# Kernel tuning notes

Hardware: AMD Instinct MI355X
Metric: run time of the kernel (lower is better)

Reference implementation:

```python
import jax, jax.numpy as jnp
import numpy as np

N_HASHES = 4
CHUNK = 144
REDUCTION = 4

# PyTorch bicubic (a=-0.75), align_corners=False, integer scale 2 ->
# fixed fractional offsets t=0.75 (even outputs) and t=0.25 (odd outputs).
_EW = jnp.array([-0.03515625, 0.26171875, 0.87890625, -0.10546875], jnp.float32)
_OW = _EW[::-1]


def _up2_axis(x, axis):
    n = x.shape[axis]
    pad = [(0, 0)] * x.ndim
    pad[axis] = (2, 2)
    xp = jnp.pad(x, pad, mode='edge')  # torch clamps border indices
    sl = lambda s: jax.lax.slice_in_dim(xp, s, s + n, axis=axis)
    even = sum(_EW[k] * sl(k) for k in range(4))
    odd = sum(_OW[k] * sl(k + 1) for k in range(4))
    out = jnp.stack([even, odd], axis=axis + 1)
    shp = list(x.shape)
    shp[axis] = 2 * n
    return out.reshape(shp)


def bicubic_up2(x):
    return _up2_axis(_up2_axis(x, 2), 3)


def conv2d(x, w, b, pad):
    y = jax.lax.conv_general_dilated(x, w, (1, 1), [(pad, pad), (pad, pad)],
                                     dimension_numbers=('NCHW', 'OIHW', 'NCHW'))
    return y + b[None, :, None, None]


def _adj(t):
    # attend to own + two adjacent buckets along chunk axis (axis=2)
    return jnp.concatenate([t, jnp.roll(t, 1, axis=2), jnp.roll(t, -1, axis=2)], axis=3)


def nlsa(x, wm, bm, wa, ba, rot):
    N, Cc, H, W = x.shape
    L = H * W
    xe = conv2d(x, wm, bm, 1).reshape(N, -1, L).transpose(0, 2, 1)  # [N,L,C]
    ye = conv2d(x, wa, ba, 0).reshape(N, -1, L).transpose(0, 2, 1)  # [N,L,C*red]
    C = xe.shape[-1]
    hash_buckets = min(L // CHUNK + (L // CHUNK) % 2, 128)
    # LSH: random rotations -> argmax bucket codes (non-differentiable, detached)
    rotated = jnp.einsum('btf,fhi->bhti', xe, rot)  # [N,h,L,hb//2]
    rotated = jnp.concatenate([rotated, -rotated], axis=-1)  # [N,h,L,hb]
    codes = jnp.argmax(rotated, axis=-1)  # [N,h,L]
    codes = codes + (jnp.arange(N_HASHES) * hash_buckets)[None, :, None]
    codes = jax.lax.stop_gradient(codes.reshape(N, -1))  # [N,h*L]
    indices = jnp.argsort(codes, axis=-1)
    undo = jnp.argsort(indices, axis=-1)
    mod = indices % L
    xs = jnp.take_along_axis(xe, mod[..., None], axis=1)  # [N,h*L,C]
    ys = jnp.take_along_axis(ye, mod[..., None], axis=1)  # [N,h*L,C*red]
    padding = (-L) % CHUNK
    xb = xs.reshape(N, N_HASHES, L, C)
    yb = ys.reshape(N, N_HASHES, L, C * REDUCTION)
    if padding:
        xb = jnp.concatenate([xb, xb[:, :, -padding:, :]], axis=2)
        yb = jnp.concatenate([yb, yb[:, :, -padding:, :]], axis=2)
    nch = xb.shape[2] // CHUNK
    xb = xb.reshape(N, N_HASHES, nch, CHUNK, C)
    yb = yb.reshape(N, N_HASHES, nch, CHUNK, C * REDUCTION)
    xm = xb / jnp.maximum(jnp.linalg.norm(xb, axis=-1, keepdims=True), 5e-5)
    xm = _adj(xm)      # [N,h,k,3*chunk,C]
    ybj = _adj(yb)     # [N,h,k,3*chunk,C*red]
    raw = jnp.einsum('bhkie,bhkje->bhkij', xb, xm)  # [N,h,k,chunk,3*chunk]
    bscore = jax.scipy.special.logsumexp(raw, axis=-1, keepdims=True)
    score = jnp.exp(raw - bscore)
    ret = jnp.einsum('bhkij,bhkje->bhkie', score, ybj)
    ret = ret.reshape(N, N_HASHES, -1, C * REDUCTION)
    bscore = bscore.reshape(N, N_HASHES, -1)
    if padding:
        ret = ret[:, :, :-padding]
        bscore = bscore[:, :, :-padding]
    ret = ret.reshape(N, -1, C * REDUCTION)
    bscore = bscore.reshape(N, -1)
    ret = jnp.take_along_axis(ret, undo[..., None], axis=1)
    bscore = jnp.take_along_axis(bscore, undo, axis=1)
    ret = ret.reshape(N, N_HASHES, L, C * REDUCTION)
    probs = jax.nn.softmax(bscore.reshape(N, N_HASHES, L, 1), axis=1)
    ret = jnp.sum(ret * probs, axis=1)  # [N,L,C*red]
    return ret.transpose(0, 2, 1).reshape(N, -1, H, W) + x


def setup_inputs() -> dict:
    key = jax.random.key(0)
    ks = jax.random.split(key, 8)
    w = lambda k, shape, fan: (jax.random.normal(k, shape, jnp.float32) / np.sqrt(fan)).astype(jnp.float32)
    return {
        'x': jax.random.normal(ks[0], (2, 64, 96, 96), jnp.float32),
        'w1': w(ks[1], (64, 64, 3, 3), 64 * 9), 'b1': jnp.zeros((64,), jnp.float32),
        'w2': w(ks[2], (64, 64, 3, 3), 64 * 9), 'b2': jnp.zeros((64,), jnp.float32),
        'wm': w(ks[3], (16, 64, 3, 3), 64 * 9), 'bm': jnp.zeros((16,), jnp.float32),
        'wa': w(ks[4], (64, 64, 1, 1), 64), 'ba': jnp.zeros((64,), jnp.float32),
        'rot': jax.random.normal(ks[5], (16, N_HASHES, 64), jnp.float32),  # [C, h, hash_buckets//2]
    }


def reference(x, w1, b1, w2, b2, wm, bm, wa, ba, rot):
    x = bicubic_up2(x)
    x = jax.nn.relu(conv2d(x, w1, b1, 1))
    x = jax.nn.relu(conv2d(x, w2, b2, 1))
    return nlsa(x, wm, bm, wa, ba, rot)
```

## Files before the change

kernel.cpp:

```cpp
#include <hip/hip_runtime.h>
#include <math.h>

#define NB 2
#define CIN 64
#define H0 96
#define W0 96
#define HH 192
#define WW 192
#define LL (HH*WW)
#define NHASH 4
#define CHK 144
#define NCHK 256
#define CE 16
#define CV 64
#define NBUCK 128
#define SEGL 576
#define NSEG 64

#define K_ROWB   80
#define V_ROWB   912
#define P_ROWB   72
#define KQ_SZB   34560
#define VT_SZB   58368
#define PST_SZB  10368
#define LKI_SZB  1728
#define QN_SZB   576
#define LDS_T1   (VT_SZB + PST_SZB + LKI_SZB)
#define LDS_T2   (KQ_SZB + VT_SZB + PST_SZB + LKI_SZB + QN_SZB)

typedef __attribute__((ext_vector_type(8))) short short8_t;
typedef __attribute__((ext_vector_type(4))) float f32x4;
union FragU { unsigned int u[4]; int4 i; short8_t s; };

__device__ __forceinline__ unsigned int cvtpk_bf16(float a, float b){
  unsigned int r;
  asm("v_cvt_pk_bf16_f32 %0, %1, %2" : "=v"(r) : "v"(a), "v"(b));
  return r;
}
__device__ __forceinline__ float bfl(unsigned int u){ return __uint_as_float(u << 16); }
__device__ __forceinline__ float bfh(unsigned int u){ return __uint_as_float(u & 0xffff0000u); }

__global__ __launch_bounds__(256) void k_upsample(const float* __restrict__ x,
                                                  float* __restrict__ out){
  int idx = blockIdx.x*256 + threadIdx.x;
  if (idx >= NB*CIN*HH*WW) return;
  int ox = idx % WW; int t2 = idx / WW;
  int oy = t2 % HH;  t2 /= HH;
  int i = oy >> 1, a = oy & 1;
  int j = ox >> 1, b = ox & 1;
  const float e0=-0.03515625f, e1=0.26171875f, e2=0.87890625f, e3=-0.10546875f;
  float wy[4], wx[4]; int ty[4], tx[4];
  if (a){ wy[0]=e3; wy[1]=e2; wy[2]=e1; wy[3]=e0; } else { wy[0]=e0; wy[1]=e1; wy[2]=e2; wy[3]=e3; }
  if (b){ wx[0]=e3; wx[1]=e2; wx[2]=e1; wx[3]=e0; } else { wx[0]=e0; wx[1]=e1; wx[2]=e2; wx[3]=e3; }
  int offy = a ? -1 : -2, offx = b ? -1 : -2;
  #pragma unroll
  for (int k=0;k<4;k++){
    int t = i + offy + k; ty[k] = t<0?0:(t>H0-1?H0-1:t);
    int s = j + offx + k; tx[k] = s<0?0:(s>W0-1?W0-1:s);
  }
  const float* xp = x + (size_t)t2*H0*W0;
  float s = 0.f;
  #pragma unroll
  for (int ky=0;ky<4;ky++){
    const float* row = xp + ty[ky]*W0;
    float rs = 0.f;
    rs = fmaf(wx[0], row[tx[0]], rs);
    rs = fmaf(wx[1], row[tx[1]], rs);
    rs = fmaf(wx[2], row[tx[2]], rs);
    rs = fmaf(wx[3], row[tx[3]], rs);
    s = fmaf(wy[ky], rs, s);
  }
  out[idx] = s;
}

__global__ __launch_bounds__(256) void k_prepw(const float* __restrict__ w,
    unsigned short* __restrict__ wsT, int CO){
  int idx = blockIdx.x*256 + threadIdx.x;
  if (idx >= CO*64*9) return;
  int tap = idx % 9; int rem = idx / 9;
  int ci = rem % 64; int co = rem / 64;
  float v = w[(size_t)(co*64 + ci)*9 + tap];
  unsigned int hu = cvtpk_bf16(v, v) & 0xffffu;
  float hf = bfl(hu);
  unsigned int lu = cvtpk_bf16(v - hf, 0.f) & 0xffffu;
  int half = ci >> 5, kg = (ci >> 3) & 3, e = ci & 7;
  size_t base = ((size_t)(tap*2 + half)*2)*CO*32 + ((size_t)co*4 + kg)*8 + e;
  wsT[base]         = (unsigned short)hu;
  wsT[base + (size_t)CO*32] = (unsigned short)lu;
}

template<int CO, bool RELU, bool OUT_NLC>
__global__ __launch_bounds__(256) void k_conv3m(const float* __restrict__ in,
    const unsigned short* __restrict__ wsT, const float* __restrict__ bias,
    float* __restrict__ out){
  __shared__ unsigned short inH[3][66][64];
  __shared__ unsigned short inL[3][66][64];
  const int t = threadIdx.x;
  const int bx = blockIdx.x, y = blockIdx.y, n = blockIdx.z;
  const int x0 = bx*64;
  const int l = t & 63, w = t >> 6;
  const int lq = l & 15, kg = l >> 4;

  for (int e = t; e < 3072; e += 256){
    const int chunk = e & 15;
    const int strip = e >> 4;
    const int ci = strip & 63, row = strip >> 6;
    const int gy = y + row - 1;
    float4 v = make_float4(0.f,0.f,0.f,0.f);
    if (gy >= 0 && gy < HH)
      v = *(const float4*)&in[(((size_t)n*CIN + ci)*HH + gy)*WW + x0 + chunk*4];
    float vv[4] = {v.x, v.y, v.z, v.w};
    #pragma unroll
    for (int j = 0; j < 4; ++j){
      const int col = 1 + chunk*4 + j;
      const int sci = (((ci >> 3) ^ (col & 7)) << 3) | (ci & 7);
      unsigned int hu = cvtpk_bf16(vv[j], vv[j]);
      unsigned int lu = cvtpk_bf16(vv[j] - bfl(hu), 0.f);
      inH[row][col][sci] = (unsigned short)hu;
      inL[row][col][sci] = (unsigned short)lu;
    }
  }
  if (t < 192){
    const int ci = t & 63, row = t >> 6;
    const int gy = y + row - 1;
    const bool okY = (gy >= 0 && gy < HH);
    const float* ip = &in[(((size_t)n*CIN + ci)*HH + (size_t)(okY?gy:0))*WW];
    float vL = (okY && x0 >= 1) ? ip[x0-1] : 0.f;
    float vR = (okY && x0+64 < WW) ? ip[x0+64] : 0.f;
    unsigned int hL = cvtpk_bf16(vL, vL);
    unsigned int lLu = cvtpk_bf16(vL - bfl(hL), 0.f);
    unsigned int hR = cvtpk_bf16(vR, vR);
    unsigned int lRu = cvtpk_bf16(vR - bfl(hR), 0.f);
    const int sci0 = ci;
    const int sci65 = (((ci >> 3) ^ 1) << 3) | (ci & 7);
    inH[row][0][sci0]  = (unsigned short)hL;  inL[row][0][sci0]  = (unsigned short)lLu;
    inH[row][65][sci65] = (unsigned short)hR; inL[row][65][sci65] = (unsigned short)lRu;
  }
  __syncthreads();

  constexpr int NCT = CO/16;
  f32x4 acc[NCT];
  #pragma unroll
  for (int c=0;c<NCT;c++) acc[c] = (f32x4){0.f,0.f,0.f,0.f};
  const unsigned short* wlane = wsT + (size_t)lq*32 + (size_t)kg*8;

  #pragma unroll
  for (int tap=0; tap<9; ++tap){
    const int ky = tap/3, kx = tap - ky*3;
    const int col = w*16 + lq + kx;
    #pragma unroll
    for (int half=0; half<2; ++half){
      const int sci = ((((half<<2) | kg) ^ (col & 7)) << 3);
      FragU Bh, Bl;
      Bh.i = *(const int4*)&inH[ky][col][sci];
      Bl.i = *(const int4*)&inL[ky][col][sci];
      const unsigned short* wth = wlane + (size_t)((tap*2+half)*2)*CO*32;
      #pragma unroll
      for (int ct=0; ct<NCT; ++ct){
        FragU Ah, Al;
        Ah.i = *(const int4*)(wth + ct*512);
        Al.i = *(const int4*)(wth + CO*32 + ct*512);
        acc[ct] = __builtin_amdgcn_mfma_f32_16x16x32_bf16(Ah.s, Bl.s, acc[ct], 0,0,0);
        acc[ct] = __builtin_amdgcn_mfma_f32_16x16x32_bf16(Al.s, Bh.s, acc[ct], 0,0,0);
        acc[ct] = __builtin_amdgcn_mfma_f32_16x16x32_bf16(Ah.s, Bh.s, acc[ct], 0,0,0);
      }
    }
  }

  const int px = x0 + w*16 + lq;
  if constexpr (!OUT_NLC){
    #pragma unroll
    for (int ct=0; ct<NCT; ++ct){
      #pragma unroll
      for (int r=0; r<4; ++r){
        const int co = ct*16 + kg*4 + r;
        float v = acc[ct][r] + bias[co];
        if (RELU) v = fmaxf(v, 0.f);
        out[(((size_t)n*CO + co)*HH + y)*WW + px] = v;
      }
    }
  } else {
    #pragma unroll
    for (int r=0; r<4; ++r){
      const int co = kg*4 + r;
      float v = acc[0][r] + bias[co];
      if (RELU) v = fmaxf(v, 0.f);
      out[((size_t)n*LL + y*WW + px)*CO + co] = v;
    }
  }
}

__global__ __launch_bounds__(256) void k_conv1x1(const float* __restrict__ x2,
    const float* __restrict__ wa, const float* __restrict__ ba,
    unsigned short* __restrict__ yeB){
  __shared__ float xs[64][64];
  __shared__ float wts[64][64];
  const int t = threadIdx.x;
  const int n = blockIdx.y;
  const int l0 = blockIdx.x*64;
  for (int e=t; e<4096; e+=256){
    int ci = e >> 6, l = e & 63;
    xs[ci][l]  = x2[((size_t)n*CIN+ci)*LL + l0 + l];
    wts[ci][l] = wa[(size_t)l*64 + ci];
  }
  __syncthreads();
  const int l = t & 63, cq = t >> 6;
  float acc[16];
  #pragma unroll
  for (int i=0;i<16;i++) acc[i] = ba[cq*16+i];
  for (int ci=0; ci<64; ci++){
    float xv = xs[ci][l];
    #pragma unroll
    for (int i=0;i<16;i++) acc[i] = fmaf(xv, wts[ci][cq*16+i], acc[i]);
  }
  unsigned int wds[8];
  #pragma unroll
  for (int i=0;i<8;i++) wds[i] = cvtpk_bf16(acc[2*i], acc[2*i+1]);
  uint4* op = (uint4*)&yeB[((size_t)n*LL + l0 + l)*64 + cq*16];
  op[0] = make_uint4(wds[0],wds[1],wds[2],wds[3]);
  op[1] = make_uint4(wds[4],wds[5],wds[6],wds[7]);
}

__global__ __launch_bounds__(128) void k_codes(const float* __restrict__ xe,
    const float* __restrict__ rot, unsigned char* __restrict__ codes){
  __shared__ float rs[NHASH][64][16];
  const int t = threadIdx.x;
  for (int e=t; e<4096; e+=128){
    int f = e >> 8; int rem = e & 255;
    int h = rem >> 6; int i = rem & 63;
    rs[h][i][f] = rot[((size_t)f*NHASH + h)*64 + i];
  }
  __syncthreads();
  const int n = blockIdx.y;
  const int l = blockIdx.x*128 + t;
  float q[16];
  const float* xr = &xe[((size_t)n*LL + l)*16];
  #pragma unroll
  for (int f=0;f<16;f++) q[f] = xr[f];
  #pragma unroll
  for (int h=0;h<NHASH;h++){
    float bp = -3.0e38f, bn = -3.0e38f; int ap=0, an=0;
    for (int i=0;i<64;i++){
      float s = 0.f;
      #pragma unroll
      for (int f=0;f<16;f++) s = fmaf(q[f], rs[h][i][f], s);
      if (s > bp){ bp = s; ap = i; }
      if (-s > bn){ bn = -s; an = i; }
    }
    int code = (bp >= bn) ? ap : (64 + an);
    codes[((size_t)n*NHASH + h)*LL + l] = (unsigned char)code;
  }
}

__global__ __launch_bounds__(256) void k_hist(const unsigned char* __restrict__ codes,
    unsigned int* __restrict__ segHist){
  __shared__ unsigned int h[NBUCK];
  const int t = threadIdx.x;
  if (t < NBUCK) h[t] = 0;
  __syncthreads();
  const int n = blockIdx.z, hh = blockIdx.y, s = blockIdx.x;
  const unsigned char* cp = codes + ((size_t)n*NHASH + hh)*LL + (size_t)s*SEGL;
  for (int e=t; e<SEGL; e+=256) atomicAdd(&h[cp[e]], 1u);
  __syncthreads();
  if (t < NBUCK)
    segHist[(((size_t)(n*NHASH+hh))*NSEG + s)*NBUCK + t] = h[t];
}

__global__ __launch_bounds__(128) void k_scan(unsigned int* __restrict__ segHist){
  __shared__ unsigned int tot[NBUCK];
  __shared__ unsigned int base[NBUCK];
  const int b = threadIdx.x;
  const size_t off = (size_t)blockIdx.x * NSEG * NBUCK;
  unsigned int run = 0;
  for (int s=0;s<NSEG;s++){
    unsigned int v = segHist[off + (size_t)s*NBUCK + b];
    segHist[off + (size_t)s*NBUCK + b] = run;
    run += v;
  }
  tot[b] = run;
  __syncthreads();
  if (b==0){ unsigned int r=0; for (int i=0;i<NBUCK;i++){ base[i]=r; r+=tot[i]; } }
  __syncthreads();
  const unsigned int bb = base[b];
  for (int s=0;s<NSEG;s++) segHist[off + (size_t)s*NBUCK + b] += bb;
}

__global__ __launch_bounds__(256) void k_rank(const unsigned char* __restrict__ codes,
    const unsigned int* __restrict__ segHist, int* __restrict__ sortPos,
    int* __restrict__ srtIdx){
  __shared__ unsigned int cw[SEGL/4];
  __shared__ unsigned int sbase[NBUCK];
  const int t = threadIdx.x;
  const int n = blockIdx.z, hh = blockIdx.y, s = blockIdx.x;
  const size_t cb = ((size_t)n*NHASH + hh)*LL + (size_t)s*SEGL;
  const unsigned int* cp32 = (const unsigned int*)(codes + cb);
  for (int e=t; e<SEGL/4; e+=256) cw[e] = cp32[e];
  if (t < NBUCK)
    sbase[t] = segHist[(((size_t)(n*NHASH+hh))*NSEG + s)*NBUCK + t];
  __syncthreads();
  const size_t ob = ((size_t)n*NHASH + hh)*LL;
  for (int e=t; e<SEGL; e+=256){
    unsigned int c = (cw[e>>2] >> ((e&3)*8)) & 0xffu;
    unsigned int mul = c * 0x01010101u;
    int cnt = 0;
    const int nw = e >> 2;
    for (int wi=0; wi<nw; wi++){
      unsigned int v = cw[wi] ^ mul;
      unsigned int t1 = (v & 0x7f7f7f7fu) + 0x7f7f7f7fu;
      unsigned int z = ~(t1 | v) & 0x80808080u;
      cnt += __popc(z);
    }
    unsigned int lastw = cw[nw];
    const int nbp = e & 3;
    for (int bp=0; bp<nbp; bp++)
      if (((lastw >> (bp*8)) & 0xffu) == c) cnt++;
    int pos = (int)sbase[c] + cnt;
    int l = s*SEGL + e;
    sortPos[ob + l] = pos;
    srtIdx[ob + pos] = l;
  }
}

__global__ __launch_bounds__(256) void k_gatherK(const float* __restrict__ xe,
    const int* __restrict__ srtIdx, unsigned short* __restrict__ Ksrt,
    float* __restrict__ normQ){
  const int idx = blockIdx.x*256 + threadIdx.x;
  if (idx >= NB*NHASH*LL) return;
  const int n = idx / (NHASH*LL);
  const int lk = srtIdx[idx];
  const float4* xr = (const float4*)&xe[((size_t)n*LL + lk)*16];
  float4 v0 = xr[0], v1 = xr[1], v2 = xr[2], v3 = xr[3];
  float f[16] = {v0.x,v0.y,v0.z,v0.w, v1.x,v1.y,v1.z,v1.w,
                 v2.x,v2.y,v2.z,v2.w, v3.x,v3.y,v3.z,v3.w};
  float ss = 0.f;
  #pragma unroll
  for (int i=0;i<16;i++) ss = fmaf(f[i], f[i], ss);
  const float nq = sqrtf(ss);
  normQ[idx] = nq;
  const float inv = 1.f / fmaxf(nq, 5e-5f);
  #pragma unroll
  for (int i=0;i<16;i++) f[i] *= inv;
  unsigned int kh[8], klo[8];
  #pragma unroll
  for (int i=0;i<8;i++) kh[i] = cvtpk_bf16(f[2*i], f[2*i+1]);
  #pragma unroll
  for (int i=0;i<8;i++)
    klo[i] = cvtpk_bf16(f[2*i] - bfl(kh[i]), f[2*i+1] - bfh(kh[i]));
  int4* kr = (int4*)(Ksrt + (size_t)idx*32);
  kr[0] = make_int4((int)kh[0],(int)kh[1],(int)kh[2],(int)kh[3]);
  kr[1] = make_int4((int)kh[4],(int)kh[5],(int)kh[6],(int)kh[7]);
  kr[2] = make_int4((int)klo[0],(int)klo[1],(int)klo[2],(int)klo[3]);
  kr[3] = make_int4((int)klo[4],(int)klo[5],(int)klo[6],(int)klo[7]);
}

template<int TIER>
__global__ __launch_bounds__(576) void k_attn2(const float* __restrict__ xe,
    const unsigned short* __restrict__ yeB, const int* __restrict__ srtIdx,
    const unsigned short* __restrict__ Ksrt, const float* __restrict__ normQ,
    unsigned short* __restrict__ retS, float* __restrict__ bscore){
  extern __shared__ char smem[];
  constexpr int KQOFF = (TIER==2) ? KQ_SZB : 0;
  unsigned short* Kq = (unsigned short*)smem;
  char* Vt  = smem + KQOFF;
  char* Pst = Vt + VT_SZB;
  int* lkI  = (int*)(Pst + PST_SZB);
  float* qn = (float*)(Pst + PST_SZB + LKI_SZB);

  const int t = threadIdx.x;
  const int k = blockIdx.x, hh = blockIdx.y, n = blockIdx.z;
  const size_t sb = ((size_t)n*NHASH + hh)*LL;
  const int l = t & 63, w = t >> 6;
  const int lq16 = l & 15, g = l >> 4;

  if (t < 432){
    const int c3 = t / CHK, jl = t - c3*CHK;
    const int kc = (c3==0) ? k : ((c3==1) ? ((k+NCHK-1)&(NCHK-1)) : ((k+1)&(NCHK-1)));
    const int lk = srtIdx[sb + (size_t)kc*CHK + jl];
    lkI[t] = lk;
    if constexpr (TIER==2){
      const float4* xr = (const float4*)&xe[((size_t)n*LL + lk)*16];
      float4 v0 = xr[0], v1 = xr[1], v2 = xr[2], v3 = xr[3];
      float f[16] = {v0.x,v0.y,v0.z,v0.w, v1.x,v1.y,v1.z,v1.w,
                     v2.x,v2.y,v2.z,v2.w, v3.x,v3.y,v3.z,v3.w};
      float ss = 0.f;
      #pragma unroll
      for (int i=0;i<16;i++) ss = fmaf(f[i], f[i], ss);
      const float nq = sqrtf(ss);
      if (c3 == 0) qn[jl] = nq;
      const float inv = 1.f / fmaxf(nq, 5e-5f);
      #pragma unroll
      for (int i=0;i<16;i++) f[i] *= inv;
      unsigned int kh[8], klo[8];
      #pragma unroll
      for (int i=0;i<8;i++) kh[i] = cvtpk_bf16(f[2*i], f[2*i+1]);
      #pragma unroll
      for (int i=0;i<8;i++)
        klo[i] = cvtpk_bf16(f[2*i] - bfl(kh[i]), f[2*i+1] - bfh(kh[i]));
      int4* kr = (int4*)((char*)Kq + t*K_ROWB);
      kr[0] = make_int4((int)kh[0],(int)kh[1],(int)kh[2],(int)kh[3]);
      kr[1] = make_int4((int)kh[4],(int)kh[5],(int)kh[6],(int)kh[7]);
      kr[2] = make_int4((int)klo[0],(int)klo[1],(int)klo[2],(int)klo[3]);
      kr[3] = make_int4((int)klo[4],(int)klo[5],(int)klo[6],(int)klo[7]);
    }
  }
  if (t < 512){
    int c = t >> 3, jp = t & 7;
    *(unsigned int*)(Vt + c*V_ROWB + 864 + jp*4) = 0u;
  }
  __syncthreads();

  #pragma unroll 4
  for (int it=0; it<24; ++it){
    const int e = t + it*576;
    const int jp = e >> 6, c = e & 63;
    const unsigned int a = yeB[((size_t)n*LL + lkI[2*jp  ])*64 + c];
    const unsigned int b = yeB[((size_t)n*LL + lkI[2*jp+1])*64 + c];
    *(unsigned int*)(Vt + c*V_ROWB + jp*4) = a | (b << 16);
  }
  const int qg = w*16 + lq16;
  const int pq = k*CHK + qg;
  FragU b1, b2;
  float nq_;
  if constexpr (TIER==1){
    const unsigned short* qrow = Ksrt + (sb + pq)*32;
    b1.i = *(const int4*)(qrow + (g&1)*8);
    if (g < 2) b2.i = *(const int4*)(qrow + 16 + (g&1)*8);
    else { b2.u[0]=0u; b2.u[1]=0u; b2.u[2]=0u; b2.u[3]=0u; }
    nq_ = normQ[sb + pq];
  } else {
    const char* qrow = (const char*)Kq + qg*K_ROWB;
    b1.i = *(const int4*)(qrow + (g&1)*16);
    if (g < 2) b2.i = *(const int4*)(qrow + 32 + (g&1)*16);
    else { b2.u[0]=0u; b2.u[1]=0u; b2.u[2]=0u; b2.u[3]=0u; }
    nq_ = qn[qg];
  }
  const float msc = fmaxf(nq_, 5e-5f);
  __syncthreads();

  float sum = 0.f;
  f32x4 O0 = {0.f,0.f,0.f,0.f}, O1 = O0, O2 = O0, O3 = O0;
  char* Pw = Pst + w*(16*P_ROWB);
  for (int u=0; u<14; ++u){
    #pragma unroll
    for (int sub=0; sub<2; ++sub){
      const int t27 = u*2 + sub;
      uint2 pw;
      if (t27 < 27){
        FragU a;
        if constexpr (TIER==1){
          const int c3 = t27 / 9;
          const int kc = (c3==0) ? k : ((c3==1) ? ((k+NCHK-1)&(NCHK-1)) : ((k+1)&(NCHK-1)));
          const int row16 = (t27 - c3*9)*16;
          a.i = *(const int4*)(Ksrt + (sb + (size_t)kc*CHK + row16 + lq16)*32 + g*8);
        } else {
          a.i = *(const int4*)((const char*)Kq + (size_t)(t27*16 + lq16)*K_ROWB + g*16);
        }
        f32x4 C = {0.f,0.f,0.f,0.f};
        C = __builtin_amdgcn_mfma_f32_16x16x32_bf16(a.s, b2.s, C, 0, 0, 0);
        C = __builtin_amdgcn_mfma_f32_16x16x32_bf16(a.s, b1.s, C, 0, 0, 0);
        const float p0 = __expf(fmaf(msc, C[0], -nq_));
        const float p1 = __expf(fmaf(msc, C[1], -nq_));
        const float p2 = __expf(fmaf(msc, C[2], -nq_));
        const float p3 = __expf(fmaf(msc, C[3], -nq_));
        sum += (p0+p1) + (p2+p3);
        pw = make_uint2(cvtpk_bf16(p0,p1), cvtpk_bf16(p2,p3));
      } else {
        pw = make_uint2(0u, 0u);
      }
      *(uint2*)(Pw + lq16*P_ROWB + sub*32 + g*8) = pw;
    }
    asm volatile("s_waitcnt lgkmcnt(0)" ::: "memory");
    __builtin_amdgcn_sched_barrier(0);
    FragU bp; bp.i = *(const int4*)(Pw + lq16*P_ROWB + g*16);
    const char* Vb = Vt + lq16*V_ROWB + u*64 + g*16;
    FragU av;
    av.i = *(const int4*)(Vb);             O0 = __builtin_amdgcn_mfma_f32_16x16x32_bf16(av.s, bp.s, O0, 0,0,0);
    av.i = *(const int4*)(Vb + 16*V_ROWB); O1 = __builtin_amdgcn_mfma_f32_16x16x32_bf16(av.s, bp.s, O1, 0,0,0);
    av.i = *(const int4*)(Vb + 32*V_ROWB); O2 = __builtin_amdgcn_mfma_f32_16x16x32_bf16(av.s, bp.s, O2, 0,0,0);
    av.i = *(const int4*)(Vb + 48*V_ROWB); O3 = __builtin_amdgcn_mfma_f32_16x16x32_bf16(av.s, bp.s, O3, 0,0,0);
  }
  sum += __shfl_xor(sum, 16);
  sum += __shfl_xor(sum, 32);
  const float linv = 1.f / sum;

  unsigned short* op = &retS[(sb + pq)*64];
  {
    uint2 s0 = make_uint2(cvtpk_bf16(O0[0]*linv, O0[1]*linv), cvtpk_bf16(O0[2]*linv, O0[3]*linv));
    uint2 s1 = make_uint2(cvtpk_bf16(O1[0]*linv, O1[1]*linv), cvtpk_bf16(O1[2]*linv, O1[3]*linv));
    uint2 s2 = make_uint2(cvtpk_bf16(O2[0]*linv, O2[1]*linv), cvtpk_bf16(O2[2]*linv, O2[3]*linv));
    uint2 s3 = make_uint2(cvtpk_bf16(O3[0]*linv, O3[1]*linv), cvtpk_bf16(O3[2]*linv, O3[3]*linv));
    *(uint2*)(op +  0 + g*4) = s0;
    *(uint2*)(op + 16 + g*4) = s1;
    *(uint2*)(op + 32 + g*4) = s2;
    *(uint2*)(op + 48 + g*4) = s3;
  }
  if (g == 0) bscore[sb + pq] = nq_ + logf(sum);
}

__global__ __launch_bounds__(256) void k_combine(const unsigned short* __restrict__ retS,
    const float* __restrict__ bscore, const int* __restrict__ sortPos,
    const float* __restrict__ x2, float* __restrict__ out){
  const int idx = blockIdx.x*256 + threadIdx.x;
  if (idx >= NB*LL) return;
  const int l = idx % LL, n = idx / LL;
  float bs[NHASH]; int pp[NHASH];
  #pragma unroll
  for (int h=0;h<NHASH;h++){
    size_t sb = ((size_t)n*NHASH + h)*LL;
    int p = sortPos[sb + l];
    pp[h] = p; bs[h] = bscore[sb + p];
  }
  float m = fmaxf(fmaxf(bs[0],bs[1]), fmaxf(bs[2],bs[3]));
  float wsum = 0.f; float wv[NHASH];
  #pragma unroll
  for (int h=0;h<NHASH;h++){ wv[h] = expf(bs[h]-m); wsum += wv[h]; }
  const float winv = 1.f / wsum;
  float o[64];
  #pragma unroll
  for (int i=0;i<64;i++) o[i]=0.f;
  #pragma unroll
  for (int h=0;h<NHASH;h++){
    const float wh = wv[h]*winv;
    const uint4* rp = (const uint4*)&retS[(((size_t)n*NHASH + h)*LL + pp[h])*64];
    #pragma unroll
    for (int i2=0;i2<8;i2++){
      uint4 v = rp[i2];
      o[i2*8+0] = fmaf(wh, bfl(v.x), o[i2*8+0]);
      o[i2*8+1] = fmaf(wh, bfh(v.x), o[i2*8+1]);
      o[i2*8+2] = fmaf(wh, bfl(v.y), o[i2*8+2]);
      o[i2*8+3] = fmaf(wh, bfh(v.y), o[i2*8+3]);
      o[i2*8+4] = fmaf(wh, bfl(v.z), o[i2*8+4]);
      o[i2*8+5] = fmaf(wh, bfh(v.z), o[i2*8+5]);
      o[i2*8+6] = fmaf(wh, bfl(v.w), o[i2*8+6]);
      o[i2*8+7] = fmaf(wh, bfh(v.w), o[i2*8+7]);
    }
  }
  #pragma unroll
  for (int c=0;c<64;c++){
    size_t oi = ((size_t)n*64 + c)*LL + l;
    out[oi] = o[c] + x2[oi];
  }
}

extern "C" void kernel_launch(void* const* d_in, const int* in_sizes, int n_in,
                              void* d_out, int out_size, void* d_ws, size_t ws_size,
                              hipStream_t stream){
  const float* x   = (const float*)d_in[0];
  const float* w1  = (const float*)d_in[1];
  const float* b1  = (const float*)d_in[2];
  const float* w2  = (const float*)d_in[3];
  const float* b2  = (const float*)d_in[4];
  const float* wm  = (const float*)d_in[5];
  const float* bm  = (const float*)d_in[6];
  const float* wa  = (const float*)d_in[7];
  const float* ba  = (const float*)d_in[8];
  const float* rot = (const float*)d_in[9];
  float* outp = (float*)d_out;
  char* ws = (char*)d_ws;
  const size_t FM   = (size_t)NB*CIN*HH*WW*sizeof(float);
  const size_t YEB  = (size_t)NB*LL*64*2;
  const size_t RETB = (size_t)NB*NHASH*LL*64*2;
  const size_t NHL4 = (size_t)NB*NHASH*LL*4;

  char* p = ws;
  unsigned short* yeB = (unsigned short*)p;  p += YEB;
  char* regA = p;                            p += RETB;
  float* x2  = (float*)p;                    p += FM;
  float* xe  = (float*)p;                    p += (size_t)NB*LL*CE*sizeof(float);
  unsigned char* codes = (unsigned char*)p;  p += (size_t)NB*NHASH*LL;
  unsigned int* segHist = (unsigned int*)p;  p += (size_t)NB*NHASH*NSEG*NBUCK*4;
  int* sortPos = (int*)p;                    p += NHL4;
  int* srtIdx  = (int*)p;                    p += NHL4;
  float* bscore = (float*)p;                 p += NHL4;
  unsigned short* wsT1 = (unsigned short*)p; p += (size_t)9*2*2*64*32*2;
  unsigned short* wsT2 = (unsigned short*)p; p += (size_t)9*2*2*64*32*2;
  unsigned short* wsTm = (unsigned short*)p; p += (size_t)9*2*2*16*32*2;
  const size_t needT2 = (size_t)(p - ws);
  unsigned short* Ksrt = (unsigned short*)p; p += (size_t)NB*NHASH*LL*32*2;
  float* normQ = (float*)p;                  p += NHL4;
  const size_t needT1 = (size_t)(p - ws);

  unsigned short* retS = (unsigned short*)regA;
  float* x0u = (float*)regA;
  float* y1  = (float*)(regA + FM);
  if (ws_size < needT2) return;
  const bool preg = (ws_size >= needT1);

  hipFuncSetAttribute((const void*)k_attn2<1>,
                      hipFuncAttributeMaxDynamicSharedMemorySize, LDS_T1);
  hipFuncSetAttribute((const void*)k_attn2<2>,
                      hipFuncAttributeMaxDynamicSharedMemorySize, LDS_T2);

  k_prepw<<<dim3((64*64*9+255)/256), dim3(256), 0, stream>>>(w1, wsT1, 64);
  k_prepw<<<dim3((64*64*9+255)/256), dim3(256), 0, stream>>>(w2, wsT2, 64);
  k_prepw<<<dim3((16*64*9+255)/256), dim3(256), 0, stream>>>(wm, wsTm, 16);
  k_upsample<<<dim3((NB*CIN*HH*WW+255)/256), dim3(256), 0, stream>>>(x, x0u);
  k_conv3m<64,true,false><<<dim3(3, HH, NB), dim3(256), 0, stream>>>(x0u, wsT1, b1, y1);
  k_conv3m<64,true,false><<<dim3(3, HH, NB), dim3(256), 0, stream>>>(y1, wsT2, b2, x2);
  k_conv3m<16,false,true><<<dim3(3, HH, NB), dim3(256), 0, stream>>>(x2, wsTm, bm, xe);
  k_conv1x1<<<dim3(LL/64, NB), dim3(256), 0, stream>>>(x2, wa, ba, yeB);
  k_codes<<<dim3(LL/128, NB), dim3(128), 0, stream>>>(xe, rot, codes);
  k_hist<<<dim3(NSEG, NHASH, NB), dim3(256), 0, stream>>>(codes, segHist);
  k_scan<<<dim3(NB*NHASH), dim3(128), 0, stream>>>(segHist);
  k_rank<<<dim3(NSEG, NHASH, NB), dim3(256), 0, stream>>>(codes, segHist, sortPos, srtIdx);
  if (preg){
    k_gatherK<<<dim3((NB*NHASH*LL+255)/256), dim3(256), 0, stream>>>(xe, srtIdx, Ksrt, normQ);
    k_attn2<1><<<dim3(NCHK, NHASH, NB), dim3(576), LDS_T1, stream>>>(
        xe, yeB, srtIdx, Ksrt, normQ, retS, bscore);
  } else {
    k_attn2<2><<<dim3(NCHK, NHASH, NB), dim3(576), LDS_T2, stream>>>(
        xe, yeB, srtIdx, Ksrt, normQ, retS, bscore);
  }
  k_combine<<<dim3((NB*LL+255)/256), dim3(256), 0, stream>>>(retS, bscore, sortPos, x2, outp);
}
```

Measured before the change: 352.3 us.

## Scatter attention outputs to original positions and double-buffer score/PV pipeline

```diff
diff --git a/kernel.cpp b/kernel.cpp
--- a/kernel.cpp
+++ b/kernel.cpp
@@ -25,8 +25,8 @@
 #define PST_SZB  10368
 #define LKI_SZB  1728
 #define QN_SZB   576
-#define LDS_T1   (VT_SZB + PST_SZB + LKI_SZB)
 #define LDS_T2   (KQ_SZB + VT_SZB + PST_SZB + LKI_SZB + QN_SZB)
+#define LDS_T1   (VT_SZB + LKI_SZB)
 
 typedef __attribute__((ext_vector_type(8))) short short8_t;
 typedef __attribute__((ext_vector_type(4))) float f32x4;
@@ -286,8 +286,7 @@
 }
 
 __global__ __launch_bounds__(256) void k_rank(const unsigned char* __restrict__ codes,
-    const unsigned int* __restrict__ segHist, int* __restrict__ sortPos,
-    int* __restrict__ srtIdx){
+    const unsigned int* __restrict__ segHist, int* __restrict__ srtIdx){
   __shared__ unsigned int cw[SEGL/4];
   __shared__ unsigned int sbase[NBUCK];
   const int t = threadIdx.x;
@@ -315,9 +314,7 @@
     for (int bp=0; bp<nbp; bp++)
       if (((lastw >> (bp*8)) & 0xffu) == c) cnt++;
     int pos = (int)sbase[c] + cnt;
-    int l = s*SEGL + e;
-    sortPos[ob + l] = pos;
-    srtIdx[ob + pos] = l;
+    srtIdx[ob + pos] = s*SEGL + e;
   }
 }
 
@@ -353,18 +350,15 @@
   kr[3] = make_int4((int)klo[4],(int)klo[5],(int)klo[6],(int)klo[7]);
 }
 
-template<int TIER>
-__global__ __launch_bounds__(576) void k_attn2(const float* __restrict__ xe,
-    const unsigned short* __restrict__ yeB, const int* __restrict__ srtIdx,
-    const unsigned short* __restrict__ Ksrt, const float* __restrict__ normQ,
-    unsigned short* __restrict__ retS, float* __restrict__ bscore){
+__global__ __launch_bounds__(576) void k_attn2t1(const unsigned short* __restrict__ yeB,
+    const int* __restrict__ srtIdx, const unsigned short* __restrict__ Ksrt,
+    const float* __restrict__ normQ, unsigned short* __restrict__ retS,
+    float* __restrict__ bscore){
   extern __shared__ char smem[];
-  constexpr int KQOFF = (TIER==2) ? KQ_SZB : 0;
-  unsigned short* Kq = (unsigned short*)smem;
-  char* Vt  = smem + KQOFF;
-  char* Pst = Vt + VT_SZB;
-  int* lkI  = (int*)(Pst + PST_SZB);
-  float* qn = (float*)(Pst + PST_SZB + LKI_SZB);
+  char* Vt  = smem;
+  int* lkI  = (int*)(smem + VT_SZB);
+  __shared__ char PstA[9][1024];
+  __shared__ char PstB[9][1024];
 
   const int t = threadIdx.x;
   const int k = blockIdx.x, hh = blockIdx.y, n = blockIdx.z;
@@ -375,33 +369,7 @@
   if (t < 432){
     const int c3 = t / CHK, jl = t - c3*CHK;
     const int kc = (c3==0) ? k : ((c3==1) ? ((k+NCHK-1)&(NCHK-1)) : ((k+1)&(NCHK-1)));
-    const int lk = srtIdx[sb + (size_t)kc*CHK + jl];
-    lkI[t] = lk;
-    if constexpr (TIER==2){
-      const float4* xr = (const float4*)&xe[((size_t)n*LL + lk)*16];
-      float4 v0 = xr[0], v1 = xr[1], v2 = xr[2], v3 = xr[3];
-      float f[16] = {v0.x,v0.y,v0.z,v0.w, v1.x,v1.y,v1.z,v1.w,
-                     v2.x,v2.y,v2.z,v2.w, v3.x,v3.y,v3.z,v3.w};
-      float ss = 0.f;
-      #pragma unroll
-      for (int i=0;i<16;i++) ss = fmaf(f[i], f[i], ss);
-      const float nq = sqrtf(ss);
-      if (c3 == 0) qn[jl] = nq;
-      const float inv = 1.f / fmaxf(nq, 5e-5f);
-      #pragma unroll
-      for (int i=0;i<16;i++) f[i] *= inv;
-      unsigned int kh[8], klo[8];
-      #pragma unroll
-      for (int i=0;i<8;i++) kh[i] = cvtpk_bf16(f[2*i], f[2*i+1]);
-      #pragma unroll
-      for (int i=0;i<8;i++)
-        klo[i] = cvtpk_bf16(f[2*i] - bfl(kh[i]), f[2*i+1] - bfh(kh[i]));
-      int4* kr = (int4*)((char*)Kq + t*K_ROWB);
-      kr[0] = make_int4((int)kh[0],(int)kh[1],(int)kh[2],(int)kh[3]);
-      kr[1] = make_int4((int)kh[4],(int)kh[5],(int)kh[6],(int)kh[7]);
-      kr[2] = make_int4((int)klo[0],(int)klo[1],(int)klo[2],(int)klo[3]);
-      kr[3] = make_int4((int)klo[4],(int)klo[5],(int)klo[6],(int)klo[7]);
-    }
+    lkI[t] = srtIdx[sb + (size_t)kc*CHK + jl];
   }
   if (t < 512){
     int c = t >> 3, jp = t & 7;
@@ -419,15 +387,166 @@
   }
   const int qg = w*16 + lq16;
   const int pq = k*CHK + qg;
+  const int lqs = lkI[qg];
+  FragU b1, b2;
+  const unsigned short* qrow = Ksrt + (sb + pq)*32;
+  b1.i = *(const int4*)(qrow + (g&1)*8);
+  if (g < 2) b2.i = *(const int4*)(qrow + 16 + (g&1)*8);
+  else { b2.u[0]=0u; b2.u[1]=0u; b2.u[2]=0u; b2.u[3]=0u; }
+  const float nq_ = normQ[sb + pq];
+  const float msc = fmaxf(nq_, 5e-5f);
+  __syncthreads();
+
+  float sum = 0.f;
+  char* const pwA = &PstA[w][0];
+  char* const pwB = &PstB[w][0];
+  const int pws = lq16*64 + (g&1)*8;
+  const int prd = lq16*64 + ((g ^ (lq16&3))<<4);
+
+  auto qksub = [&](int u, char* __restrict__ pw){
+    #pragma unroll
+    for (int sub=0; sub<2; ++sub){
+      const int t27 = 2*u + sub;
+      uint2 pwv;
+      if (t27 < 27){
+        const int c3 = t27 / 9;
+        const int kc = (c3==0) ? k : ((c3==1) ? ((k+NCHK-1)&(NCHK-1)) : ((k+1)&(NCHK-1)));
+        const int row16 = (t27 - c3*9)*16;
+        FragU a; a.i = *(const int4*)(Ksrt + (sb + (size_t)kc*CHK + row16 + lq16)*32 + g*8);
+        f32x4 C = {0.f,0.f,0.f,0.f};
+        C = __builtin_amdgcn_mfma_f32_16x16x32_bf16(a.s, b2.s, C, 0, 0, 0);
+        C = __builtin_amdgcn_mfma_f32_16x16x32_bf16(a.s, b1.s, C, 0, 0, 0);
+        const float p0 = __expf(fmaf(msc, C[0], -nq_));
+        const float p1 = __expf(fmaf(msc, C[1], -nq_));
+        const float p2 = __expf(fmaf(msc, C[2], -nq_));
+        const float p3 = __expf(fmaf(msc, C[3], -nq_));
+        sum += (p0+p1) + (p2+p3);
+        pwv = make_uint2(cvtpk_bf16(p0,p1), cvtpk_bf16(p2,p3));
+      } else {
+        pwv = make_uint2(0u, 0u);
+      }
+      const int chunk = (sub*2 + (g>>1)) ^ (lq16 & 3);
+      *(uint2*)(pw + pws + (chunk<<4)) = pwv;
+    }
+  };
+
+  f32x4 O0 = {0.f,0.f,0.f,0.f}, O1 = O0, O2 = O0, O3 = O0;
+  qksub(0, pwA);
+  #pragma unroll
+  for (int uu=0; uu<7; ++uu){
+    {
+      const int u = 2*uu;
+      const char* Vb = Vt + lq16*V_ROWB + u*64 + g*16;
+      FragU av0, av1, av2, av3;
+      av0.i = *(const int4*)(Vb);
+      av1.i = *(const int4*)(Vb + 16*V_ROWB);
+      av2.i = *(const int4*)(Vb + 32*V_ROWB);
+      av3.i = *(const int4*)(Vb + 48*V_ROWB);
+      qksub(u+1, pwB);
+      FragU bp; bp.i = *(const int4*)(pwA + prd);
+      O0 = __builtin_amdgcn_mfma_f32_16x16x32_bf16(av0.s, bp.s, O0, 0,0,0);
+      O1 = __builtin_amdgcn_mfma_f32_16x16x32_bf16(av1.s, bp.s, O1, 0,0,0);
+      O2 = __builtin_amdgcn_mfma_f32_16x16x32_bf16(av2.s, bp.s, O2, 0,0,0);
+      O3 = __builtin_amdgcn_mfma_f32_16x16x32_bf16(av3.s, bp.s, O3, 0,0,0);
+    }
+    {
+      const int u = 2*uu + 1;
+      const char* Vb = Vt + lq16*V_ROWB + u*64 + g*16;
+      FragU av0, av1, av2, av3;
+      av0.i = *(const int4*)(Vb);
+      av1.i = *(const int4*)(Vb + 16*V_ROWB);
+      av2.i = *(const int4*)(Vb + 32*V_ROWB);
+      av3.i = *(const int4*)(Vb + 48*V_ROWB);
+      qksub(u+1, pwA);
+      FragU bp; bp.i = *(const int4*)(pwB + prd);
+      O0 = __builtin_amdgcn_mfma_f32_16x16x32_bf16(av0.s, bp.s, O0, 0,0,0);
+      O1 = __builtin_amdgcn_mfma_f32_16x16x32_bf16(av1.s, bp.s, O1, 0,0,0);
+      O2 = __builtin_amdgcn_mfma_f32_16x16x32_bf16(av2.s, bp.s, O2, 0,0,0);
+      O3 = __builtin_amdgcn_mfma_f32_16x16x32_bf16(av3.s, bp.s, O3, 0,0,0);
+    }
+  }
+  sum += __shfl_xor(sum, 16);
+  sum += __shfl_xor(sum, 32);
+  const float linv = 1.f / sum;
+
+  unsigned short* op = &retS[(sb + lqs)*64];
+  {
+    uint2 s0 = make_uint2(cvtpk_bf16(O0[0]*linv, O0[1]*linv), cvtpk_bf16(O0[2]*linv, O0[3]*linv));
+    uint2 s1 = make_uint2(cvtpk_bf16(O1[0]*linv, O1[1]*linv), cvtpk_bf16(O1[2]*linv, O1[3]*linv));
+    uint2 s2 = make_uint2(cvtpk_bf16(O2[0]*linv, O2[1]*linv), cvtpk_bf16(O2[2]*linv, O2[3]*linv));
+    uint2 s3 = make_uint2(cvtpk_bf16(O3[0]*linv, O3[1]*linv), cvtpk_bf16(O3[2]*linv, O3[3]*linv));
+    *(uint2*)(op +  0 + g*4) = s0;
+    *(uint2*)(op + 16 + g*4) = s1;
+    *(uint2*)(op + 32 + g*4) = s2;
+    *(uint2*)(op + 48 + g*4) = s3;
+  }
+  if (g == 0) bscore[sb + lqs] = nq_ + logf(sum);
+}
+
+__global__ __launch_bounds__(576) void k_attn2b(const float* __restrict__ xe,
+    const unsigned short* __restrict__ yeB, const int* __restrict__ srtIdx,
+    unsigned short* __restrict__ retS, float* __restrict__ bscore){
+  extern __shared__ char smem[];
+  unsigned short* Kq = (unsigned short*)smem;
+  char* Vt  = smem + KQ_SZB;
+  char* Pst = Vt + VT_SZB;
+  int* lkI  = (int*)(Pst + PST_SZB);
+  float* qn = (float*)(Pst + PST_SZB + LKI_SZB);
+
+  const int t = threadIdx.x;
+  const int k = blockIdx.x, hh = blockIdx.y, n = blockIdx.z;
+  const size_t sb = ((size_t)n*NHASH + hh)*LL;
+  const int l = t & 63, w = t >> 6;
+  const int lq16 = l & 15, g = l >> 4;
+
+  if (t < 432){
+    const int c3 = t / CHK, jl = t - c3*CHK;
+    const int kc = (c3==0) ? k : ((c3==1) ? ((k+NCHK-1)&(NCHK-1)) : ((k+1)&(NCHK-1)));
+    const int lk = srtIdx[sb + (size_t)kc*CHK + jl];
+    lkI[t] = lk;
+    const float4* xr = (const float4*)&xe[((size_t)n*LL + lk)*16];
+    float4 v0 = xr[0], v1 = xr[1], v2 = xr[2], v3 = xr[3];
+    float f[16] = {v0.x,v0.y,v0.z,v0.w, v1.x,v1.y,v1.z,v1.w,
+                   v2.x,v2.y,v2.z,v2.w, v3.x,v3.y,v3.z,v3.w};
+    float ss = 0.f;
+    #pragma unroll
+    for (int i=0;i<16;i++) ss = fmaf(f[i], f[i], ss);
+    const float nq = sqrtf(ss);
+    if (c3 == 0) qn[jl] = nq;
+    const float inv = 1.f / fmaxf(nq, 5e-5f);
+    #pragma unroll
+    for (int i=0;i<16;i++) f[i] *= inv;
+    unsigned int kh[8], klo[8];
+    #pragma unroll
+    for (int i=0;i<8;i++) kh[i] = cvtpk_bf16(f[2*i], f[2*i+1]);
+    #pragma unroll
+    for (int i=0;i<8;i++)
+      klo[i] = cvtpk_bf16(f[2*i] - bfl(kh[i]), f[2*i+1] - bfh(kh[i]));
+    int4* kr = (int4*)((char*)Kq + t*K_ROWB);
+    kr[0] = make_int4((int)kh[0],(int)kh[1],(int)kh[2],(int)kh[3]);
+    kr[1] = make_int4((int)kh[4],(int)kh[5],(int)kh[6],(int)kh[7]);
+    kr[2] = make_int4((int)klo[0],(int)klo[1],(int)klo[2],(int)klo[3]);
+    kr[3] = make_int4((int)klo[4],(int)klo[5],(int)klo[6],(int)klo[7]);
+  }
+  if (t < 512){
+    int c = t >> 3, jp = t & 7;
+    *(unsigned int*)(Vt + c*V_ROWB + 864 + jp*4) = 0u;
+  }
+  __syncthreads();
+
+  #pragma unroll 4
+  for (int it=0; it<24; ++it){
+    const int e = t + it*576;
+    const int jp = e >> 6, c = e & 63;
+    const unsigned int a = yeB[((size_t)n*LL + lkI[2*jp  ])*64 + c];
+    const unsigned int b = yeB[((size_t)n*LL + lkI[2*jp+1])*64 + c];
+    *(unsigned int*)(Vt + c*V_ROWB + jp*4) = a | (b << 16);
+  }
+  const int qg = w*16 + lq16;
+  const int lqs = lkI[qg];
   FragU b1, b2;
   float nq_;
-  if constexpr (TIER==1){
-    const unsigned short* qrow = Ksrt + (sb + pq)*32;
-    b1.i = *(const int4*)(qrow + (g&1)*8);
-    if (g < 2) b2.i = *(const int4*)(qrow + 16 + (g&1)*8);
-    else { b2.u[0]=0u; b2.u[1]=0u; b2.u[2]=0u; b2.u[3]=0u; }
-    nq_ = normQ[sb + pq];
-  } else {
+  {
     const char* qrow = (const char*)Kq + qg*K_ROWB;
     b1.i = *(const int4*)(qrow + (g&1)*16);
     if (g < 2) b2.i = *(const int4*)(qrow + 32 + (g&1)*16);
@@ -447,14 +566,7 @@
       uint2 pw;
       if (t27 < 27){
         FragU a;
-        if constexpr (TIER==1){
-          const int c3 = t27 / 9;
-          const int kc = (c3==0) ? k : ((c3==1) ? ((k+NCHK-1)&(NCHK-1)) : ((k+1)&(NCHK-1)));
-          const int row16 = (t27 - c3*9)*16;
-          a.i = *(const int4*)(Ksrt + (sb + (size_t)kc*CHK + row16 + lq16)*32 + g*8);
-        } else {
-          a.i = *(const int4*)((const char*)Kq + (size_t)(t27*16 + lq16)*K_ROWB + g*16);
-        }
+        a.i = *(const int4*)((const char*)Kq + (size_t)(t27*16 + lq16)*K_ROWB + g*16);
         f32x4 C = {0.f,0.f,0.f,0.f};
         C = __builtin_amdgcn_mfma_f32_16x16x32_bf16(a.s, b2.s, C, 0, 0, 0);
         C = __builtin_amdgcn_mfma_f32_16x16x32_bf16(a.s, b1.s, C, 0, 0, 0);
@@ -483,7 +595,7 @@
   sum += __shfl_xor(sum, 32);
   const float linv = 1.f / sum;
 
-  unsigned short* op = &retS[(sb + pq)*64];
+  unsigned short* op = &retS[(sb + lqs)*64];
   {
     uint2 s0 = make_uint2(cvtpk_bf16(O0[0]*linv, O0[1]*linv), cvtpk_bf16(O0[2]*linv, O0[3]*linv));
     uint2 s1 = make_uint2(cvtpk_bf16(O1[0]*linv, O1[1]*linv), cvtpk_bf16(O1[2]*linv, O1[3]*linv));
@@ -494,22 +606,19 @@
     *(uint2*)(op + 32 + g*4) = s2;
     *(uint2*)(op + 48 + g*4) = s3;
   }
-  if (g == 0) bscore[sb + pq] = nq_ + logf(sum);
+  if (g == 0) bscore[sb + lqs] = nq_ + logf(sum);
 }
 
 __global__ __launch_bounds__(256) void k_combine(const unsigned short* __restrict__ retS,
-    const float* __restrict__ bscore, const int* __restrict__ sortPos,
-    const float* __restrict__ x2, float* __restrict__ out){
+    const float* __restrict__ bscore, const float* __restrict__ x2,
+    float* __restrict__ out){
   const int idx = blockIdx.x*256 + threadIdx.x;
   if (idx >= NB*LL) return;
   const int l = idx % LL, n = idx / LL;
-  float bs[NHASH]; int pp[NHASH];
-  #pragma unroll
-  for (int h=0;h<NHASH;h++){
-    size_t sb = ((size_t)n*NHASH + h)*LL;
-    int p = sortPos[sb + l];
-    pp[h] = p; bs[h] = bscore[sb + p];
-  }
+  float bs[NHASH];
+  #pragma unroll
+  for (int h=0;h<NHASH;h++)
+    bs[h] = bscore[((size_t)n*NHASH + h)*LL + l];
   float m = fmaxf(fmaxf(bs[0],bs[1]), fmaxf(bs[2],bs[3]));
   float wsum = 0.f; float wv[NHASH];
   #pragma unroll
@@ -521,7 +630,7 @@
   #pragma unroll
   for (int h=0;h<NHASH;h++){
     const float wh = wv[h]*winv;
-    const uint4* rp = (const uint4*)&retS[(((size_t)n*NHASH + h)*LL + pp[h])*64];
+    const uint4* rp = (const uint4*)&retS[(((size_t)n*NHASH + h)*LL + l)*64];
     #pragma unroll
     for (int i2=0;i2<8;i2++){
       uint4 v = rp[i2];
@@ -569,7 +678,6 @@
   float* xe  = (float*)p;                    p += (size_t)NB*LL*CE*sizeof(float);
   unsigned char* codes = (unsigned char*)p;  p += (size_t)NB*NHASH*LL;
   unsigned int* segHist = (unsigned int*)p;  p += (size_t)NB*NHASH*NSEG*NBUCK*4;
-  int* sortPos = (int*)p;                    p += NHL4;
   int* srtIdx  = (int*)p;                    p += NHL4;
   float* bscore = (float*)p;                 p += NHL4;
   unsigned short* wsT1 = (unsigned short*)p; p += (size_t)9*2*2*64*32*2;
@@ -586,9 +694,9 @@
   if (ws_size < needT2) return;
   const bool preg = (ws_size >= needT1);
 
-  hipFuncSetAttribute((const void*)k_attn2<1>,
+  hipFuncSetAttribute((const void*)k_attn2t1,
                       hipFuncAttributeMaxDynamicSharedMemorySize, LDS_T1);
-  hipFuncSetAttribute((const void*)k_attn2<2>,
+  hipFuncSetAttribute((const void*)k_attn2b,
                       hipFuncAttributeMaxDynamicSharedMemorySize, LDS_T2);
 
   k_prepw<<<dim3((64*64*9+255)/256), dim3(256), 0, stream>>>(w1, wsT1, 64);
@@ -602,14 +710,14 @@
   k_codes<<<dim3(LL/128, NB), dim3(128), 0, stream>>>(xe, rot, codes);
   k_hist<<<dim3(NSEG, NHASH, NB), dim3(256), 0, stream>>>(codes, segHist);
   k_scan<<<dim3(NB*NHASH), dim3(128), 0, stream>>>(segHist);
-  k_rank<<<dim3(NSEG, NHASH, NB), dim3(256), 0, stream>>>(codes, segHist, sortPos, srtIdx);
+  k_rank<<<dim3(NSEG, NHASH, NB), dim3(256), 0, stream>>>(codes, segHist, srtIdx);
   if (preg){
     k_gatherK<<<dim3((NB*NHASH*LL+255)/256), dim3(256), 0, stream>>>(xe, srtIdx, Ksrt, normQ);
-    k_attn2<1><<<dim3(NCHK, NHASH, NB), dim3(576), LDS_T1, stream>>>(
-        xe, yeB, srtIdx, Ksrt, normQ, retS, bscore);
+    k_attn2t1<<<dim3(NCHK, NHASH, NB), dim3(576), LDS_T1, stream>>>(
+        yeB, srtIdx, Ksrt, normQ, retS, bscore);
   } else {
-    k_attn2<2><<<dim3(NCHK, NHASH, NB), dim3(576), LDS_T2, stream>>>(
-        xe, yeB, srtIdx, Ksrt, normQ, retS, bscore);
-  }
-  k_combine<<<dim3((NB*LL+255)/256), dim3(256), 0, stream>>>(retS, bscore, sortPos, x2, outp);
-}
+    k_attn2b<<<dim3(NCHK, NHASH, NB), dim3(576), LDS_T2, stream>>>(
+        xe, yeB, srtIdx, retS, bscore);
+  }
+  k_combine<<<dim3((NB*LL+255)/256), dim3(256), 0, stream>>>(retS, bscore, x2, outp);
+}
```

New measurement: 392.2 us. 11.3% more time.
